# Optimization experiments

Measured on AMD Instinct MI355X. Metric: run time of the kernel, lower is better.

## Reference

```python
import jax, jax.numpy as jnp
import numpy as np

CHUNK = 32
NUM_HEADS = 4
HEAD_K = 256
HEAD_V = 256
EPS = 1e-05


def l2norm(x, eps=1e-6):
    return x * jax.lax.rsqrt(jnp.sum(x * x, axis=-1, keepdims=True) + eps)


def causal_depthwise_conv(x, w):
    # x: [b, l, d], w: [d, K]; causal depthwise conv1d (left pad K-1)
    K = w.shape[1]
    l = x.shape[1]
    xp = jnp.pad(x, ((0, 0), (K - 1, 0), (0, 0)))
    return sum(w[:, k] * xp[:, k:k + l, :] for k in range(K))


def delta_rule_chunkwise(q, k, v, beta):
    # q,k: [b,h,l,dk], v: [b,h,l,dv], beta: [b,h,l]; l divisible by CHUNK
    b, h, l, dk = q.shape
    dv = v.shape[-1]
    c = CHUNK
    n = l // c
    q = l2norm(q)
    k = l2norm(k)
    v = v * beta[..., None]
    k_beta = k * beta[..., None]
    resh = lambda x: x.reshape(b, h, n, c, x.shape[-1])
    q, k, v, k_beta = map(resh, (q, k, v, k_beta))
    tri_strict = jnp.tril(jnp.ones((c, c), dtype=q.dtype), -1)  # strictly lower
    attn = -(k_beta @ jnp.swapaxes(k, -1, -2)) * tri_strict  # [b,h,n,c,c]

    def body(i, a):
        # a[i, :i] += sum_j a[i, j] * a[j, :i]; zero elsewhere by structure
        row = a[..., i, :]  # [b,h,n,c]
        upd = jnp.einsum('bhnj,bhnjk->bhnk', row, a)
        return a.at[..., i, :].add(upd)

    attn = jax.lax.fori_loop(1, c, body, attn)
    attn = attn + jnp.eye(c, dtype=attn.dtype)
    u = attn @ v        # [b,h,n,c,dv]
    w = attn @ k_beta   # [b,h,n,c,dk]

    mask_causal = jnp.tril(jnp.ones((c, c), dtype=q.dtype), 0)  # incl diag
    S0 = jnp.zeros((b, h, dk, dv), dtype=q.dtype)
    to_front = lambda x: jnp.moveaxis(x, 2, 0)  # [n,b,h,c,d]

    def step(S, inp):
        q_i, k_i, u_i, w_i = inp
        attn_i = (q_i @ jnp.swapaxes(k_i, -1, -2)) * mask_causal
        u_new = u_i - w_i @ S
        o_i = q_i @ S + attn_i @ u_new
        S = S + jnp.swapaxes(k_i, -1, -2) @ u_new
        return S, o_i

    S, o = jax.lax.scan(step, S0, (to_front(q), to_front(k), to_front(u), to_front(w)))
    o = jnp.moveaxis(o, 0, 2).reshape(b, h, l, dv)
    return o, S


def setup_inputs() -> dict:
    key = jax.random.key(0)
    ks = jax.random.split(key, 12)
    b, l, d = 4, 4096, 1024
    sc = 0.02
    return {
        'hidden_states': jax.random.normal(ks[0], (b, l, d), jnp.float32),
        'Wq': jax.random.normal(ks[1], (1024, 1024), jnp.float32) * sc,
        'Wk': jax.random.normal(ks[2], (1024, 1024), jnp.float32) * sc,
        'Wv': jax.random.normal(ks[3], (1024, 1024), jnp.float32) * sc,
        'conv_q': jax.random.normal(ks[4], (1024, 4), jnp.float32) * 0.1,
        'conv_k': jax.random.normal(ks[5], (1024, 4), jnp.float32) * 0.1,
        'conv_v': jax.random.normal(ks[6], (1024, 4), jnp.float32) * 0.1,
        'Wb': jax.random.normal(ks[7], (4, 1024), jnp.float32) * sc,
        'Wmix': jax.random.normal(ks[8], (4, 1024), jnp.float32) * sc,
        'norm_w': jnp.ones((256,), jnp.float32),
        'Wo': jax.random.normal(ks[9], (1024, 1024), jnp.float32) * sc,
    }


def reference(hidden_states, Wq, Wk, Wv, conv_q, conv_k, conv_v, Wb, Wmix, norm_w, Wo):
    x = hidden_states
    b, l, d = x.shape
    h, dk, dv = NUM_HEADS, HEAD_K, HEAD_V
    # projections + depthwise causal short conv + silu
    q = jax.nn.silu(causal_depthwise_conv(x @ Wq.T, conv_q))
    k = jax.nn.silu(causal_depthwise_conv(x @ Wk.T, conv_k))
    v = jax.nn.silu(causal_depthwise_conv(x @ Wv.T, conv_v))
    v_token = v.reshape(b, l, h, dv)
    qh = q.reshape(b, l, h, dk).transpose(0, 2, 1, 3)
    kh = k.reshape(b, l, h, dk).transpose(0, 2, 1, 3)
    vh = v_token.transpose(0, 2, 1, 3)
    beta = jax.nn.sigmoid(x @ Wb.T).transpose(0, 2, 1)  # [b,h,l]
    o, S = delta_rule_chunkwise(qh, kh, vh, beta)
    o = o.transpose(0, 2, 1, 3)  # [b,l,h,dv]
    mix = jax.nn.sigmoid(x @ Wmix.T)[..., None]  # [b,l,h,1]
    o = mix * o + (1.0 - mix) * v_token
    # per-head RMSNorm
    o = o * jax.lax.rsqrt(jnp.mean(o * o, axis=-1, keepdims=True) + EPS) * norm_w
    o = o.reshape(b, l, h * dv) @ Wo.T
    return o
```

## Files before the change

kernel.cpp:

```cpp
#include <hip/hip_runtime.h>
#include <hip/hip_bf16.h>

typedef __hip_bfloat16 bf16;
typedef unsigned short u16;
typedef __attribute__((ext_vector_type(4))) float f32x4;
typedef __attribute__((ext_vector_type(8))) short bf16x8;
typedef __attribute__((ext_vector_type(2))) unsigned int u32x2;

#define MFMA16(a, b, c) __builtin_amdgcn_mfma_f32_16x16x32_bf16((a), (b), (c), 0, 0, 0)

__device__ __forceinline__ float bfu2f(u16 u){
  return __uint_as_float(((unsigned int)u) << 16);
}
__device__ __forceinline__ u16 f2bfu(float x){
  return __builtin_bit_cast(u16, __float2bfloat16(x));
}
__device__ __forceinline__ void gload16(const void* g, const void* l){
  __builtin_amdgcn_global_load_lds(
      (const __attribute__((address_space(1))) unsigned int*)g,
      (__attribute__((address_space(3))) unsigned int*)l, 16, 0, 0);
}

__global__ __launch_bounds__(256) void cvt_bf16(
    const float* __restrict__ src, u16* __restrict__ dst, int n8)
{
  int i = blockIdx.x * 256 + threadIdx.x;
  if (i >= n8) return;
  const float4* s = (const float4*)src;
  float4 a = s[i * 2], b = s[i * 2 + 1];
  u16 o[8] = {f2bfu(a.x), f2bfu(a.y), f2bfu(a.z), f2bfu(a.w),
              f2bfu(b.x), f2bfu(b.y), f2bfu(b.z), f2bfu(b.w)};
  *(bf16x8*)(dst + (size_t)i * 8) = *(bf16x8*)o;
}

template<int NMAT, bool F32OUT>
__global__ __launch_bounds__(256) void gemm_bt(
    const u16* __restrict__ A,
    const u16* __restrict__ B0, const u16* __restrict__ B1, const u16* __restrict__ B2,
    void* __restrict__ C0, void* __restrict__ C1, void* __restrict__ C2)
{
  const u16* B; void* C;
  if (NMAT == 1 || blockIdx.z == 0){ B = B0; C = C0; }
  else if (blockIdx.z == 1)        { B = B1; C = C1; }
  else                             { B = B2; C = C2; }
  __shared__ char lds[2][2][16384];
  const int tid = threadIdx.x;
  const int lane = tid & 63, wv = tid >> 6;
  const int lc = lane & 15, lh = lane >> 4;
  const int wr = wv >> 1, wc = wv & 1;
  const int m0 = blockIdx.x * 128, n0 = blockIdx.y * 128;

  f32x4 acc[4][4];
  #pragma unroll
  for (int mt = 0; mt < 4; mt++)
    #pragma unroll
    for (int nt = 0; nt < 4; nt++) acc[mt][nt] = (f32x4){0.f, 0.f, 0.f, 0.f};

  auto stage = [&](int buf, int k0){
    #pragma unroll
    for (int c = 0; c < 4; c++){
      const int q = wv * 4096 + c * 1024;
      const int row = (q >> 7) + (lane >> 3);
      const int slot = (lane & 7) ^ (row & 7);
      gload16(A + (size_t)(m0 + row) * 1024 + k0 + slot * 8, &lds[buf][0][q]);
      gload16(B + (size_t)(n0 + row) * 1024 + k0 + slot * 8, &lds[buf][1][q]);
    }
  };

  stage(0, 0);
  __syncthreads();
  int cur = 0;
  for (int t = 0; t < 16; t++){
    if (t < 15) stage(cur ^ 1, (t + 1) * 64);
    const char* Abuf = lds[cur][0];
    const char* Bbuf = lds[cur][1];
    #pragma unroll
    for (int kk = 0; kk < 2; kk++){
      bf16x8 af[4], bfr[4];
      #pragma unroll
      for (int mt = 0; mt < 4; mt++){
        int r = wr * 64 + mt * 16 + lc;
        int slot = (kk * 4 + lh) ^ (r & 7);
        af[mt] = *(const bf16x8*)(const void*)(Abuf + r * 128 + slot * 16);
      }
      #pragma unroll
      for (int nt = 0; nt < 4; nt++){
        int r = wc * 64 + nt * 16 + lc;
        int slot = (kk * 4 + lh) ^ (r & 7);
        bfr[nt] = *(const bf16x8*)(const void*)(Bbuf + r * 128 + slot * 16);
      }
      #pragma unroll
      for (int mt = 0; mt < 4; mt++)
        #pragma unroll
        for (int nt = 0; nt < 4; nt++)
          acc[mt][nt] = MFMA16(af[mt], bfr[nt], acc[mt][nt]);
    }
    __syncthreads();
    cur ^= 1;
  }

  #pragma unroll
  for (int mt = 0; mt < 4; mt++)
    #pragma unroll
    for (int nt = 0; nt < 4; nt++)
      #pragma unroll
      for (int rg = 0; rg < 4; rg++){
        int row = m0 + wr * 64 + mt * 16 + lh * 4 + rg;
        int col = n0 + wc * 64 + nt * 16 + lc;
        if (F32OUT) ((float*)C)[(size_t)row * 1024 + col] = acc[mt][nt][rg];
        else ((bf16*)C)[(size_t)row * 1024 + col] = __float2bfloat16(acc[mt][nt][rg]);
      }
}

__global__ __launch_bounds__(256) void small_proj(
    const float* __restrict__ x, const float* __restrict__ Wb,
    const float* __restrict__ Wmix, float* __restrict__ beta, float* __restrict__ mixb)
{
  const int tok = blockIdx.x;
  const int tid = threadIdx.x;
  __shared__ __align__(16) float xrow[1024];
  ((float4*)xrow)[tid] = ((const float4*)(x + (size_t)tok * 1024))[tid];
  __syncthreads();
  const int o = tid >> 5, g = tid & 31;
  const float* Wrow = (o < 4) ? (Wb + (size_t)o * 1024) : (Wmix + (size_t)(o - 4) * 1024);
  float p = 0.f;
  for (int e = g; e < 256; e += 32){
    float4 xv = ((const float4*)xrow)[e];
    float4 wv = ((const float4*)Wrow)[e];
    p += xv.x * wv.x + xv.y * wv.y + xv.z * wv.z + xv.w * wv.w;
  }
  for (int off = 16; off; off >>= 1) p += __shfl_down(p, off, 32);
  if (g == 0){
    float s = 1.f / (1.f + expf(-p));
    int b = tok >> 12, t = tok & 4095;
    if (o < 4) beta[((size_t)(b * 4 + o)) * 4096 + t] = s;
    else       mixb[(size_t)tok * 4 + (o - 4)] = s;
  }
}

__global__ __launch_bounds__(256) void conv_silu3(
    const bf16* __restrict__ in0, const bf16* __restrict__ in1, const bf16* __restrict__ in2,
    const float* __restrict__ w0, const float* __restrict__ w1, const float* __restrict__ w2,
    bf16* __restrict__ o0, bf16* __restrict__ o1, bf16* __restrict__ o2)
{
  const bf16* in; const float* wc; bf16* out;
  if (blockIdx.y == 0)      { in = in0; wc = w0; out = o0; }
  else if (blockIdx.y == 1) { in = in1; wc = w1; out = o1; }
  else                      { in = in2; wc = w2; out = o2; }
  const int idx8 = blockIdx.x * 256 + threadIdx.x;
  const int c8 = (idx8 & 127) * 8;
  const int tt = idx8 >> 7;
  const int t  = tt & 4095;
  const u16* inu = (const u16*)in;
  const size_t base = (size_t)tt * 1024 + c8;
  bf16x8 zv = {0, 0, 0, 0, 0, 0, 0, 0};
  bf16x8 x3 = *(const bf16x8*)(const void*)(inu + base);
  bf16x8 x2 = (t >= 1) ? *(const bf16x8*)(const void*)(inu + base - 1024) : zv;
  bf16x8 x1 = (t >= 2) ? *(const bf16x8*)(const void*)(inu + base - 2048) : zv;
  bf16x8 x0 = (t >= 3) ? *(const bf16x8*)(const void*)(inu + base - 3072) : zv;
  u16 o8[8];
  #pragma unroll
  for (int e = 0; e < 8; e++){
    const float4 w4 = ((const float4*)wc)[c8 + e];
    float s = w4.w * bfu2f((u16)x3[e]) + w4.z * bfu2f((u16)x2[e])
            + w4.y * bfu2f((u16)x1[e]) + w4.x * bfu2f((u16)x0[e]);
    s = s / (1.f + expf(-s));
    o8[e] = f2bfu(s);
  }
  *(bf16x8*)(void*)((u16*)out + base) = *(bf16x8*)o8;
}

__global__ __launch_bounds__(256, 2) void chunk_prep(
    bf16* __restrict__ qc, const bf16* __restrict__ kc, const bf16* __restrict__ vc,
    const float* __restrict__ beta,
    bf16* __restrict__ u_out, bf16* __restrict__ w_out,
    bf16* __restrict__ Ab, bf16* __restrict__ kTg)
{
  __shared__ char kS[16384], qS[16384];
  __shared__ float att[1056];
  __shared__ char Th[2048], Tl[2048];
  __shared__ char vTh[8192], vTl[8192];
  __shared__ char wTh[8192], wTl[8192];
  __shared__ float rnk_s[32], rnq_s[32], bvec[32];

  const int g = blockIdx.x;
  const int ch = g & 127, h = (g >> 7) & 3, b = g >> 9;
  const int tid = threadIdx.x;
  const int l = tid & 63, wv = tid >> 6;
  const int lc = l & 15, lh = l >> 4;
  const int i = tid >> 3, s = tid & 7;
  const size_t rowbase = ((size_t)(b * 4096 + ch * 32)) * 1024 + (size_t)h * 256;
  const u16* kcu = (const u16*)kc;
  const u16* qcu = (const u16*)qc;
  const u16* vcu = (const u16*)vc;

  bf16x8 kr[4], qr[4], vr[4];
  float ssk = 0.f, ssq = 0.f;
  #pragma unroll
  for (int j4 = 0; j4 < 4; j4++){
    size_t eo = rowbase + (size_t)i * 1024 + s * 32 + j4 * 8;
    kr[j4] = *(const bf16x8*)(const void*)(kcu + eo);
    qr[j4] = *(const bf16x8*)(const void*)(qcu + eo);
    vr[j4] = *(const bf16x8*)(const void*)(vcu + eo);
    #pragma unroll
    for (int e = 0; e < 8; e++){
      float kv = bfu2f((u16)kr[j4][e]); ssk += kv * kv;
      float qv = bfu2f((u16)qr[j4][e]); ssq += qv * qv;
    }
  }
  #pragma unroll
  for (int off = 1; off < 8; off <<= 1){
    ssk += __shfl_xor(ssk, off, 64);
    ssq += __shfl_xor(ssq, off, 64);
  }
  if (s == 0){
    rnk_s[i] = 1.0f / sqrtf(ssk + 1e-6f);
    rnq_s[i] = 1.0f / sqrtf(ssq + 1e-6f);
  }
  if (tid < 32) bvec[tid] = beta[((size_t)(b * 4 + h)) * 4096 + ch * 32 + tid];
  __syncthreads();

  const float rk = rnk_s[i], rq = rnq_s[i], bi = bvec[i];
  #pragma unroll
  for (int j4 = 0; j4 < 4; j4++){
    u16 kn8[8], qn8[8];
    #pragma unroll
    for (int e = 0; e < 8; e++){
      kn8[e] = f2bfu(bfu2f((u16)kr[j4][e]) * rk);
      qn8[e] = f2bfu(bfu2f((u16)qr[j4][e]) * rq);
    }
    int byt = (i * 512 + s * 64 + j4 * 16) ^ ((i & 7) << 4);
    *(bf16x8*)(void*)(kS + byt) = *(bf16x8*)kn8;
    *(bf16x8*)(void*)(qS + byt) = *(bf16x8*)qn8;
    *(bf16x8*)(void*)((u16*)qc + rowbase + (size_t)i * 1024 + s * 32 + j4 * 8) = *(bf16x8*)kn8 * 0 + *(bf16x8*)qn8;
  }
  if ((s >> 2) == 0){
    #pragma unroll
    for (int j4 = 0; j4 < 4; j4++)
      #pragma unroll
      for (int e = 0; e < 8; e++){
        int dl = (s & 3) * 32 + j4 * 8 + e;
        float vb = bfu2f((u16)vr[j4][e]) * bi;
        float kb = bfu2f((u16)kr[j4][e]) * rk * bi;
        u16 vh = f2bfu(vb), kh = f2bfu(kb);
        u16 vlo = f2bfu(vb - bfu2f(vh)), klo = f2bfu(kb - bfu2f(kh));
        int byt = dl * 64 + (((i >> 3) ^ ((dl >> 1) & 3)) << 4) + (i & 7) * 2;
        *(u16*)(vTh + byt) = vh; *(u16*)(vTl + byt) = vlo;
        *(u16*)(wTh + byt) = kh; *(u16*)(wTl + byt) = klo;
      }
  }
  __syncthreads();

  {
    const int mq = wv >> 1, nq = wv & 1;
    const int rowA = mq * 16 + lc, rowB = nq * 16 + lc;
    const int swA = (rowA & 7) << 4, swB = (rowB & 7) << 4;
    f32x4 accL = (f32x4){0.f, 0.f, 0.f, 0.f};
    f32x4 accA = (f32x4){0.f, 0.f, 0.f, 0.f};
    #pragma unroll
    for (int kt = 0; kt < 8; kt++){
      bf16x8 af  = *(const bf16x8*)(const void*)(kS + ((rowA * 512 + kt * 64 + lh * 16) ^ swA));
      bf16x8 bf_ = *(const bf16x8*)(const void*)(kS + ((rowB * 512 + kt * 64 + lh * 16) ^ swB));
      bf16x8 aq  = *(const bf16x8*)(const void*)(qS + ((rowA * 512 + kt * 64 + lh * 16) ^ swA));
      accL = MFMA16(af, bf_, accL);
      accA = MFMA16(aq, bf_, accA);
    }
    #pragma unroll
    for (int r = 0; r < 4; r++){
      int rr = mq * 16 + lh * 4 + r, cc = nq * 16 + lc;
      att[rr * 33 + cc] = (cc < rr) ? (-bvec[rr] * accL[r]) : 0.f;
      float av = (cc <= rr) ? accA[r] : 0.f;
      ((u16*)Ab)[(size_t)g * 1024 + rr * 32 + cc] = f2bfu(av);
    }
  }
  {
    u16 tmp[32];
    #pragma unroll
    for (int i2 = 0; i2 < 32; i2++)
      tmp[i2] = *(const u16*)(kS + ((i2 * 512 + tid * 2) ^ ((i2 & 7) << 4)));
    #pragma unroll
    for (int j4 = 0; j4 < 4; j4++)
      *(bf16x8*)(void*)((u16*)kTg + (size_t)g * 8192 + tid * 32 + j4 * 8) = *(bf16x8*)(tmp + j4 * 8);
  }
  __syncthreads();

  if (wv == 0 && l < 32){
    for (int ii = 1; ii < 32; ii++){
      float upd = 0.f;
      for (int m = 0; m < ii; m++)
        upd += att[ii * 33 + m] * att[m * 33 + l];
      att[ii * 33 + l] += upd;
    }
    att[l * 33 + l] = 1.0f;
  }
  __syncthreads();

  #pragma unroll
  for (int z = 0; z < 4; z++){
    int e = tid * 4 + z;
    int row = e >> 5, col = e & 31;
    float f = att[row * 33 + col];
    u16 hh = f2bfu(f), llo = f2bfu(f - bfu2f(hh));
    int byt = row * 64 + ((((col >> 3)) ^ ((row >> 1) & 3)) << 4) + (col & 7) * 2;
    *(u16*)(Th + byt) = hh; *(u16*)(Tl + byt) = llo;
  }
  __syncthreads();

  {
    const int mq = wv >> 1, nsel = wv & 1;
    const int rowA = mq * 16 + lc;
    const int sa = (lh ^ ((rowA >> 1) & 3)) << 4;
    bf16x8 ta = *(const bf16x8*)(const void*)(Th + rowA * 64 + sa);
    bf16x8 tl = *(const bf16x8*)(const void*)(Tl + rowA * 64 + sa);
    #pragma unroll
    for (int half = 0; half < 2; half++){
      if (half == 1){
        __syncthreads();
        if ((s >> 2) == 1){
          #pragma unroll
          for (int j4 = 0; j4 < 4; j4++)
            #pragma unroll
            for (int e = 0; e < 8; e++){
              int dl = (s & 3) * 32 + j4 * 8 + e;
              float vb = bfu2f((u16)vr[j4][e]) * bi;
              float kb = bfu2f((u16)kr[j4][e]) * rk * bi;
              u16 vh = f2bfu(vb), kh = f2bfu(kb);
              u16 vlo = f2bfu(vb - bfu2f(vh)), klo = f2bfu(kb - bfu2f(kh));
              int byt = dl * 64 + (((i >> 3) ^ ((dl >> 1) & 3)) << 4) + (i & 7) * 2;
              *(u16*)(vTh + byt) = vh; *(u16*)(vTl + byt) = vlo;
              *(u16*)(wTh + byt) = kh; *(u16*)(wTl + byt) = klo;
            }
        }
        __syncthreads();
      }
      #pragma unroll
      for (int nt = 0; nt < 4; nt++){
        int nl = nsel * 64 + nt * 16;
        int rowB = nl + lc;
        int sb = (lh ^ ((rowB >> 1) & 3)) << 4;
        bf16x8 bh_ = *(const bf16x8*)(const void*)(vTh + rowB * 64 + sb);
        bf16x8 bl_ = *(const bf16x8*)(const void*)(vTl + rowB * 64 + sb);
        f32x4 aU = (f32x4){0.f, 0.f, 0.f, 0.f};
        aU = MFMA16(ta, bh_, aU);
        aU = MFMA16(ta, bl_, aU);
        aU = MFMA16(tl, bh_, aU);
        bf16x8 wh_ = *(const bf16x8*)(const void*)(wTh + rowB * 64 + sb);
        bf16x8 wl_ = *(const bf16x8*)(const void*)(wTl + rowB * 64 + sb);
        f32x4 aW = (f32x4){0.f, 0.f, 0.f, 0.f};
        aW = MFMA16(ta, wh_, aW);
        aW = MFMA16(ta, wl_, aW);
        aW = MFMA16(tl, wh_, aW);
        #pragma unroll
        for (int r = 0; r < 4; r++){
          int row = mq * 16 + lh * 4 + r, col = half * 128 + nl + lc;
          ((u16*)u_out)[rowbase + (size_t)row * 1024 + col] = f2bfu(aU[r]);
          ((u16*)w_out)[rowbase + (size_t)row * 1024 + col] = f2bfu(aW[r]);
        }
      }
    }
  }
}

__global__ __launch_bounds__(128, 1) void scan_kernel(
    const u16* __restrict__ w_in, const u16* __restrict__ qn,
    const u16* __restrict__ u_in, const bf16* __restrict__ Ab,
    const bf16* __restrict__ kTg, bf16* __restrict__ o_out)
{
  extern __shared__ char smem[];
  char* wqbuf  = smem;
  char* stbuf  = smem + 65536;
  char* untbuf = smem + 81920;

  const int tid = threadIdx.x;
  const int l = tid & 63, wv = tid >> 6;
  const int lc = l & 15, lh = l >> 4;
  const int wg = blockIdx.x;
  const int bh = (wg & 7) * 2 + ((wg >> 3) & 1);
  const int vb = wg >> 4;
  const int h = bh & 3, b = bh >> 2;
  const int c0 = vb * 16;
  const int mw = wv * 16;

  f32x4 Sf[8];
  #pragma unroll
  for (int mt = 0; mt < 8; mt++) Sf[mt] = (f32x4){0.f, 0.f, 0.f, 0.f};

  const size_t bhElem = (size_t)b * 4096 * 1024 + (size_t)h * 256;
  const u16* kTu = (const u16*)kTg;

  auto stageWQ = [&](int buf, size_t rowE){
    char* wbase = wqbuf + buf * 32768 + wv * 8192;
    #pragma unroll
    for (int p = 0; p < 8; p++){
      int i = wv * 16 + p * 2 + (l >> 5);
      int logc = (l & 31) ^ (i & 7);
      size_t src = rowE + (size_t)i * 1024 + (size_t)logc * 8;
      gload16(w_in + src, wbase + p * 1024);
      gload16(qn  + src, wbase + 16384 + p * 1024);
    }
  };

  stageWQ(0, bhElem);
  for (int e = tid; e < 4096; e += 128) ((unsigned int*)(void*)stbuf)[e] = 0u;
  u16 cu0 = u_in[bhElem + (size_t)(mw + lh*4 + 0) * 1024 + c0 + lc];
  u16 cu1 = u_in[bhElem + (size_t)(mw + lh*4 + 1) * 1024 + c0 + lc];
  u16 cu2 = u_in[bhElem + (size_t)(mw + lh*4 + 2) * 1024 + c0 + lc];
  u16 cu3 = u_in[bhElem + (size_t)(mw + lh*4 + 3) * 1024 + c0 + lc];
  bf16x8 cAf = *(const bf16x8*)(const void*)(Ab + (size_t)(bh * 128) * 1024 + (mw + lc) * 32 + lh * 8);
  __syncthreads();

  int cur = 0;
  for (int ch = 0; ch < 128; ch++){
    const size_t rowElem = bhElem + (size_t)ch * 32768;
    if (ch < 127) stageWQ(cur ^ 1, rowElem + 32768);
    bf16x8 kF[8];
    {
      const size_t ktCur = (size_t)(bh * 128 + ch) * 8192;
      #pragma unroll
      for (int mt = 0; mt < 8; mt++){
        int rowK = wv * 128 + mt * 16 + lc;
        kF[mt] = *(const bf16x8*)(const void*)(kTu + ktCur + (size_t)rowK * 32 + lh * 8);
      }
    }
    u16 pu0, pu1, pu2, pu3; bf16x8 pAf;
    if (ch < 127){
      const size_t rowN = rowElem + 32768;
      pu0 = u_in[rowN + (size_t)(mw + lh*4 + 0) * 1024 + c0 + lc];
      pu1 = u_in[rowN + (size_t)(mw + lh*4 + 1) * 1024 + c0 + lc];
      pu2 = u_in[rowN + (size_t)(mw + lh*4 + 2) * 1024 + c0 + lc];
      pu3 = u_in[rowN + (size_t)(mw + lh*4 + 3) * 1024 + c0 + lc];
      pAf = *(const bf16x8*)(const void*)(Ab + (size_t)(bh * 128 + ch + 1) * 1024 + (mw + lc) * 32 + lh * 8);
    }

    const char* wl = wqbuf + cur * 32768;
    const char* ql = wl + 16384;

    f32x4 aU0 = (f32x4){0.f,0.f,0.f,0.f}, aU1 = (f32x4){0.f,0.f,0.f,0.f};
    f32x4 aO0 = (f32x4){0.f,0.f,0.f,0.f}, aO1 = (f32x4){0.f,0.f,0.f,0.f};
    {
      const int rowA = mw + lc;
      const int swA = (rowA & 7) << 4;
      const int swS = (lc & 7) << 4;
      #pragma unroll
      for (int kt = 0; kt < 8; kt++){
        const int kb = kt * 64 + lh * 16;
        bf16x8 aw = *(const bf16x8*)(const void*)(wl + ((rowA * 512 + kb) ^ swA));
        bf16x8 aq = *(const bf16x8*)(const void*)(ql + ((rowA * 512 + kb) ^ swA));
        bf16x8 sh = *(const bf16x8*)(const void*)(stbuf + ((lc * 512 + kb) ^ swS));
        bf16x8 sl = *(const bf16x8*)(const void*)(stbuf + 8192 + ((lc * 512 + kb) ^ swS));
        if (kt & 1){
          aU1 = MFMA16(aw, sh, aU1);
          aU1 = MFMA16(aw, sl, aU1);
          aO1 = MFMA16(aq, sh, aO1);
          aO1 = MFMA16(aq, sl, aO1);
        } else {
          aU0 = MFMA16(aw, sh, aU0);
          aU0 = MFMA16(aw, sl, aU0);
          aO0 = MFMA16(aq, sh, aO0);
          aO0 = MFMA16(aq, sl, aO0);
        }
      }
    }
    f32x4 accO = aO0 + aO1;
    {
      f32x4 accU = aU0 + aU1;
      float v0 = bfu2f(cu0) - accU[0];
      float v1 = bfu2f(cu1) - accU[1];
      float v2 = bfu2f(cu2) - accU[2];
      float v3 = bfu2f(cu3) - accU[3];
      u16 h0 = f2bfu(v0), h1 = f2bfu(v1), h2 = f2bfu(v2), h3 = f2bfu(v3);
      u16 l0 = f2bfu(v0 - bfu2f(h0)), l1 = f2bfu(v1 - bfu2f(h1));
      u16 l2 = f2bfu(v2 - bfu2f(h2)), l3 = f2bfu(v3 - bfu2f(h3));
      unsigned int ph0 = (unsigned)h0 | ((unsigned)h1 << 16), ph1 = (unsigned)h2 | ((unsigned)h3 << 16);
      unsigned int pl0 = (unsigned)l0 | ((unsigned)l1 << 16), pl1 = (unsigned)l2 | ((unsigned)l3 << 16);
      int off = lc * 80 + (mw + lh * 4) * 2;
      *(u32x2*)(void*)(untbuf + off)        = (u32x2){ph0, ph1};
      *(u32x2*)(void*)(untbuf + 1280 + off) = (u32x2){pl0, pl1};
    }
    __syncthreads();

    bf16x8 uh = *(const bf16x8*)(const void*)(untbuf + lc * 80 + lh * 16);
    bf16x8 ul = *(const bf16x8*)(const void*)(untbuf + 1280 + lc * 80 + lh * 16);
    accO = MFMA16(cAf, uh, accO);
    accO = MFMA16(cAf, ul, accO);
    o_out[rowElem + (size_t)(mw + lh*4 + 0) * 1024 + c0 + lc] = __float2bfloat16(accO[0]);
    o_out[rowElem + (size_t)(mw + lh*4 + 1) * 1024 + c0 + lc] = __float2bfloat16(accO[1]);
    o_out[rowElem + (size_t)(mw + lh*4 + 2) * 1024 + c0 + lc] = __float2bfloat16(accO[2]);
    o_out[rowElem + (size_t)(mw + lh*4 + 3) * 1024 + c0 + lc] = __float2bfloat16(accO[3]);

    #pragma unroll
    for (int mt = 0; mt < 8; mt++){
      Sf[mt] = MFMA16(kF[mt], uh, Sf[mt]);
      Sf[mt] = MFMA16(kF[mt], ul, Sf[mt]);
    }

    #pragma unroll
    for (int mt = 0; mt < 8; mt++){
      const int dbase = wv * 128 + mt * 16 + lh * 4;
      float v0 = Sf[mt][0], v1 = Sf[mt][1], v2 = Sf[mt][2], v3 = Sf[mt][3];
      u16 h0 = f2bfu(v0), h1 = f2bfu(v1), h2 = f2bfu(v2), h3 = f2bfu(v3);
      u16 s0 = f2bfu(v0 - bfu2f(h0)), s1 = f2bfu(v1 - bfu2f(h1));
      u16 s2 = f2bfu(v2 - bfu2f(h2)), s3 = f2bfu(v3 - bfu2f(h3));
      int off = ((lc * 512 + dbase * 2) ^ ((lc & 7) << 4));
      *(u32x2*)(void*)(stbuf + off) =
          (u32x2){(unsigned)h0 | ((unsigned)h1 << 16), (unsigned)h2 | ((unsigned)h3 << 16)};
      *(u32x2*)(void*)(stbuf + 8192 + off) =
          (u32x2){(unsigned)s0 | ((unsigned)s1 << 16), (unsigned)s2 | ((unsigned)s3 << 16)};
    }
    if (ch < 127){
      cu0 = pu0; cu1 = pu1; cu2 = pu2; cu3 = pu3; cAf = pAf;
    }
    __syncthreads();
    cur ^= 1;
  }
}

__global__ __launch_bounds__(256) void postproc(
    const bf16* __restrict__ o_in, const bf16* __restrict__ v_tok,
    const float* __restrict__ mixb, const float* __restrict__ norm_w,
    bf16* __restrict__ onorm)
{
  const int blk = blockIdx.x;
  const int d = threadIdx.x;
  const size_t gg = (size_t)blk * 256 + d;
  float ov = __bfloat162float(o_in[gg]);
  float vv = __bfloat162float(v_tok[gg]);
  float m = mixb[blk];
  float val = m * ov + (1.f - m) * vv;
  float ss = val * val;
  for (int off = 32; off; off >>= 1) ss += __shfl_down(ss, off, 64);
  __shared__ float wsum[4];
  if ((d & 63) == 0) wsum[d >> 6] = ss;
  __syncthreads();
  float tot = wsum[0] + wsum[1] + wsum[2] + wsum[3];
  float r = rsqrtf(tot * (1.f / 256.f) + 1e-5f);
  onorm[gg] = __float2bfloat16(val * r * norm_w[d]);
}

extern "C" void kernel_launch(void* const* d_in, const int* in_sizes, int n_in,
                              void* d_out, int out_size, void* d_ws, size_t ws_size,
                              hipStream_t stream)
{
  (void)in_sizes; (void)n_in; (void)out_size; (void)ws_size;
  const float* x     = (const float*)d_in[0];
  const float* Wq    = (const float*)d_in[1];
  const float* Wk    = (const float*)d_in[2];
  const float* Wv    = (const float*)d_in[3];
  const float* convq = (const float*)d_in[4];
  const float* convk = (const float*)d_in[5];
  const float* convv = (const float*)d_in[6];
  const float* Wb    = (const float*)d_in[7];
  const float* Wmix  = (const float*)d_in[8];
  const float* normw = (const float*)d_in[9];
  const float* Wo    = (const float*)d_in[10];
  float* out = (float*)d_out;

  char* wsb = (char*)d_ws;
  const size_t BIGB = (size_t)16777216 * 2;
  bf16* b0 = (bf16*)(wsb + 0*BIGB);
  bf16* b1 = (bf16*)(wsb + 1*BIGB);
  bf16* b2 = (bf16*)(wsb + 2*BIGB);
  bf16* b3 = (bf16*)(wsb + 3*BIGB);
  bf16* b4 = (bf16*)(wsb + 4*BIGB);
  bf16* b5 = (bf16*)(wsb + 5*BIGB);
  bf16*  Ab   = (bf16*) (wsb + 6*BIGB);
  float* beta = (float*)(wsb + 6*BIGB + 4194304);
  float* mixb = beta + 65536;
  bf16*  kTg  = (bf16*) (wsb + 6*BIGB + 4194304 + 524288);

  u16* xbf = (u16*)b4;
  u16* wqb = (u16*)b3;
  u16* wkb = wqb + (size_t)1024*1024;
  u16* wvb = wkb + (size_t)1024*1024;
  u16* wob = (u16*)kTg;

  cvt_bf16<<<8192, 256, 0, stream>>>(x, xbf, 2097152);
  cvt_bf16<<<512, 256, 0, stream>>>(Wq, wqb, 131072);
  cvt_bf16<<<512, 256, 0, stream>>>(Wk, wkb, 131072);
  cvt_bf16<<<512, 256, 0, stream>>>(Wv, wvb, 131072);

  gemm_bt<3, false><<<dim3(128, 8, 3), 256, 0, stream>>>(
      xbf, wqb, wkb, wvb, (void*)b0, (void*)b1, (void*)b2);
  small_proj<<<16384, 256, 0, stream>>>(x, Wb, Wmix, beta, mixb);
  conv_silu3<<<dim3(8192, 3), 256, 0, stream>>>(
      b0, b1, b2, convq, convk, convv, b3, b4, b5);
  chunk_prep<<<2048, 256, 0, stream>>>(b3, b4, b5, beta, b2, b0, Ab, kTg);
  hipFuncSetAttribute((const void*)scan_kernel,
                      hipFuncAttributeMaxDynamicSharedMemorySize, 84480);
  scan_kernel<<<256, 128, 84480, stream>>>((const u16*)b0, (const u16*)b3,
                                           (const u16*)b2, Ab, kTg, b1);
  cvt_bf16<<<512, 256, 0, stream>>>(Wo, wob, 131072);
  postproc  <<<65536, 256, 0, stream>>>(b1, b5, mixb, normw, b3);
  gemm_bt<1, true><<<dim3(128, 8, 1), 256, 0, stream>>>(
      (const u16*)b3, wob, wob, wob, (void*)out, (void*)out, (void*)out);
}
```

Baseline: 660.0 us.

## Repartition scan kernel: each wave owns 8 value columns with full state

The chunk scan now launches 64 workgroups of 8 waves instead of 256 workgroups of 2 waves. Each wave owns an 8-column slice of the value dimension and keeps the full 256-row state slice in registers, staging its state in a private LDS region. This removes the mid-chunk block barrier that exchanged u_new between waves; only the end-of-chunk barrier remains. In exchange, half of each 16-wide MFMA tile is wasted on padding (lanes with lc>=8 are idle) and register pressure doubles. Fewer workgroups also means far fewer CUs are used.

```diff
diff --git a/kernel.cpp b/kernel.cpp
--- a/kernel.cpp
+++ b/kernel.cpp
@@ -361,154 +361,178 @@
   }
 }
 
-__global__ __launch_bounds__(128, 1) void scan_kernel(
+__global__ __launch_bounds__(512, 2) void scan_kernel(
     const u16* __restrict__ w_in, const u16* __restrict__ qn,
     const u16* __restrict__ u_in, const bf16* __restrict__ Ab,
     const bf16* __restrict__ kTg, bf16* __restrict__ o_out)
 {
   extern __shared__ char smem[];
-  char* wqbuf  = smem;
-  char* stbuf  = smem + 65536;
-  char* untbuf = smem + 81920;
+  char* wqbuf = smem;
+  char* stbuf = smem + 65536;
+  char* unbuf = smem + 135168;
 
   const int tid = threadIdx.x;
   const int l = tid & 63, wv = tid >> 6;
   const int lc = l & 15, lh = l >> 4;
   const int wg = blockIdx.x;
   const int bh = (wg & 7) * 2 + ((wg >> 3) & 1);
-  const int vb = wg >> 4;
+  const int qb = wg >> 4;
   const int h = bh & 3, b = bh >> 2;
-  const int c0 = vb * 16;
-  const int mw = wv * 16;
-
-  f32x4 Sf[8];
-  #pragma unroll
-  for (int mt = 0; mt < 8; mt++) Sf[mt] = (f32x4){0.f, 0.f, 0.f, 0.f};
+  const int c0 = qb * 64 + wv * 8;
+
+  char* stw = stbuf + wv * 8704;
+  char* unw = unbuf + wv * 1280;
+
+  f32x4 Sf[16];
+  #pragma unroll
+  for (int mt = 0; mt < 16; mt++) Sf[mt] = (f32x4){0.f, 0.f, 0.f, 0.f};
 
   const size_t bhElem = (size_t)b * 4096 * 1024 + (size_t)h * 256;
   const u16* kTu = (const u16*)kTg;
 
   auto stageWQ = [&](int buf, size_t rowE){
-    char* wbase = wqbuf + buf * 32768 + wv * 8192;
-    #pragma unroll
-    for (int p = 0; p < 8; p++){
-      int i = wv * 16 + p * 2 + (l >> 5);
-      int logc = (l & 31) ^ (i & 7);
+    char* base = wqbuf + buf * 32768;
+    #pragma unroll
+    for (int s2 = 0; s2 < 2; s2++){
+      const int seg = wv * 2 + s2;
+      const int i = seg * 2 + (l >> 5);
+      const int logc = (l & 31) ^ (i & 7);
       size_t src = rowE + (size_t)i * 1024 + (size_t)logc * 8;
-      gload16(w_in + src, wbase + p * 1024);
-      gload16(qn  + src, wbase + 16384 + p * 1024);
+      gload16(w_in + src, base + seg * 1024);
+      gload16(qn  + src, base + 16384 + seg * 1024);
     }
   };
 
   stageWQ(0, bhElem);
-  for (int e = tid; e < 4096; e += 128) ((unsigned int*)(void*)stbuf)[e] = 0u;
-  u16 cu0 = u_in[bhElem + (size_t)(mw + lh*4 + 0) * 1024 + c0 + lc];
-  u16 cu1 = u_in[bhElem + (size_t)(mw + lh*4 + 1) * 1024 + c0 + lc];
-  u16 cu2 = u_in[bhElem + (size_t)(mw + lh*4 + 2) * 1024 + c0 + lc];
-  u16 cu3 = u_in[bhElem + (size_t)(mw + lh*4 + 3) * 1024 + c0 + lc];
-  bf16x8 cAf = *(const bf16x8*)(const void*)(Ab + (size_t)(bh * 128) * 1024 + (mw + lc) * 32 + lh * 8);
+  for (int e = tid; e < 19968; e += 512) ((unsigned int*)(void*)stbuf)[e] = 0u;
+  u16 cu[2][4]; bf16x8 cAf[2];
+  #pragma unroll
+  for (int mb = 0; mb < 2; mb++){
+    #pragma unroll
+    for (int r = 0; r < 4; r++)
+      cu[mb][r] = u_in[bhElem + (size_t)(mb*16 + lh*4 + r) * 1024 + c0 + (lc & 7)];
+    cAf[mb] = *(const bf16x8*)(const void*)(Ab + (size_t)(bh * 128) * 1024 + (mb*16 + lc) * 32 + lh * 8);
+  }
   __syncthreads();
 
   int cur = 0;
   for (int ch = 0; ch < 128; ch++){
     const size_t rowElem = bhElem + (size_t)ch * 32768;
-    if (ch < 127) stageWQ(cur ^ 1, rowElem + 32768);
-    bf16x8 kF[8];
+    u16 pu[2][4]; bf16x8 pAf[2];
+    if (ch < 127){
+      const size_t rowN = rowElem + 32768;
+      stageWQ(cur ^ 1, rowN);
+      #pragma unroll
+      for (int mb = 0; mb < 2; mb++){
+        #pragma unroll
+        for (int r = 0; r < 4; r++)
+          pu[mb][r] = u_in[rowN + (size_t)(mb*16 + lh*4 + r) * 1024 + c0 + (lc & 7)];
+        pAf[mb] = *(const bf16x8*)(const void*)(Ab + (size_t)(bh * 128 + ch + 1) * 1024 + (mb*16 + lc) * 32 + lh * 8);
+      }
+    }
+
+    const char* wl = wqbuf + cur * 32768;
+    const char* ql = wl + 16384;
+
+    f32x4 accU[2], accO[2];
+    #pragma unroll
+    for (int mb = 0; mb < 2; mb++){
+      accU[mb] = (f32x4){0.f,0.f,0.f,0.f};
+      accO[mb] = (f32x4){0.f,0.f,0.f,0.f};
+    }
+    {
+      const int colS = lc & 7;
+      #pragma unroll
+      for (int kt = 0; kt < 8; kt++){
+        const int dby = (kt * 64 + lh * 16) ^ (colS << 4);
+        bf16x8 sh = *(const bf16x8*)(const void*)(stw + colS * 544 + dby);
+        bf16x8 sl = *(const bf16x8*)(const void*)(stw + 4352 + colS * 544 + dby);
+        #pragma unroll
+        for (int mb = 0; mb < 2; mb++){
+          const int rowA = mb * 16 + lc;
+          const int swA = (rowA & 7) << 4;
+          bf16x8 aw = *(const bf16x8*)(const void*)(wl + ((rowA * 512 + kt * 64 + lh * 16) ^ swA));
+          bf16x8 aq = *(const bf16x8*)(const void*)(ql + ((rowA * 512 + kt * 64 + lh * 16) ^ swA));
+          accU[mb] = MFMA16(aw, sh, accU[mb]);
+          accU[mb] = MFMA16(aw, sl, accU[mb]);
+          accO[mb] = MFMA16(aq, sh, accO[mb]);
+          accO[mb] = MFMA16(aq, sl, accO[mb]);
+        }
+      }
+    }
+    if (lc < 8){
+      #pragma unroll
+      for (int mb = 0; mb < 2; mb++){
+        float v0 = bfu2f(cu[mb][0]) - accU[mb][0];
+        float v1 = bfu2f(cu[mb][1]) - accU[mb][1];
+        float v2 = bfu2f(cu[mb][2]) - accU[mb][2];
+        float v3 = bfu2f(cu[mb][3]) - accU[mb][3];
+        u16 h0 = f2bfu(v0), h1 = f2bfu(v1), h2 = f2bfu(v2), h3 = f2bfu(v3);
+        u16 l0 = f2bfu(v0 - bfu2f(h0)), l1 = f2bfu(v1 - bfu2f(h1));
+        u16 l2 = f2bfu(v2 - bfu2f(h2)), l3 = f2bfu(v3 - bfu2f(h3));
+        int off = lc * 80 + (mb * 16 + lh * 4) * 2;
+        *(u32x2*)(void*)(unw + off) =
+            (u32x2){(unsigned)h0 | ((unsigned)h1 << 16), (unsigned)h2 | ((unsigned)h3 << 16)};
+        *(u32x2*)(void*)(unw + 640 + off) =
+            (u32x2){(unsigned)l0 | ((unsigned)l1 << 16), (unsigned)l2 | ((unsigned)l3 << 16)};
+      }
+    }
+    asm volatile("" ::: "memory");
+    bf16x8 uh = *(const bf16x8*)(const void*)(unw + (lc & 7) * 80 + lh * 16);
+    bf16x8 ul = *(const bf16x8*)(const void*)(unw + 640 + (lc & 7) * 80 + lh * 16);
+
+    #pragma unroll
+    for (int mb = 0; mb < 2; mb++){
+      accO[mb] = MFMA16(cAf[mb], uh, accO[mb]);
+      accO[mb] = MFMA16(cAf[mb], ul, accO[mb]);
+    }
+    if (lc < 8){
+      #pragma unroll
+      for (int mb = 0; mb < 2; mb++)
+        #pragma unroll
+        for (int r = 0; r < 4; r++)
+          o_out[rowElem + (size_t)(mb*16 + lh*4 + r) * 1024 + c0 + lc] = __float2bfloat16(accO[mb][r]);
+    }
+
     {
       const size_t ktCur = (size_t)(bh * 128 + ch) * 8192;
       #pragma unroll
-      for (int mt = 0; mt < 8; mt++){
-        int rowK = wv * 128 + mt * 16 + lc;
-        kF[mt] = *(const bf16x8*)(const void*)(kTu + ktCur + (size_t)rowK * 32 + lh * 8);
-      }
-    }
-    u16 pu0, pu1, pu2, pu3; bf16x8 pAf;
+      for (int half = 0; half < 2; half++){
+        bf16x8 kF[8];
+        #pragma unroll
+        for (int mt = 0; mt < 8; mt++){
+          int rowK = half * 128 + mt * 16 + lc;
+          kF[mt] = *(const bf16x8*)(const void*)(kTu + ktCur + (size_t)rowK * 32 + lh * 8);
+        }
+        #pragma unroll
+        for (int mt = 0; mt < 8; mt++){
+          Sf[half*8 + mt] = MFMA16(kF[mt], uh, Sf[half*8 + mt]);
+          Sf[half*8 + mt] = MFMA16(kF[mt], ul, Sf[half*8 + mt]);
+        }
+      }
+    }
+
+    if (lc < 8){
+      #pragma unroll
+      for (int mt = 0; mt < 16; mt++){
+        float v0 = Sf[mt][0], v1 = Sf[mt][1], v2 = Sf[mt][2], v3 = Sf[mt][3];
+        u16 h0 = f2bfu(v0), h1 = f2bfu(v1), h2 = f2bfu(v2), h3 = f2bfu(v3);
+        u16 s0 = f2bfu(v0 - bfu2f(h0)), s1 = f2bfu(v1 - bfu2f(h1));
+        u16 s2 = f2bfu(v2 - bfu2f(h2)), s3 = f2bfu(v3 - bfu2f(h3));
+        int dby = (mt * 32 + lh * 8) ^ (lc << 4);
+        *(u32x2*)(void*)(stw + lc * 544 + dby) =
+            (u32x2){(unsigned)h0 | ((unsigned)h1 << 16), (unsigned)h2 | ((unsigned)h3 << 16)};
+        *(u32x2*)(void*)(stw + 4352 + lc * 544 + dby) =
+            (u32x2){(unsigned)s0 | ((unsigned)s1 << 16), (unsigned)s2 | ((unsigned)s3 << 16)};
+      }
+    }
     if (ch < 127){
-      const size_t rowN = rowElem + 32768;
-      pu0 = u_in[rowN + (size_t)(mw + lh*4 + 0) * 1024 + c0 + lc];
-      pu1 = u_in[rowN + (size_t)(mw + lh*4 + 1) * 1024 + c0 + lc];
-      pu2 = u_in[rowN + (size_t)(mw + lh*4 + 2) * 1024 + c0 + lc];
-      pu3 = u_in[rowN + (size_t)(mw + lh*4 + 3) * 1024 + c0 + lc];
-      pAf = *(const bf16x8*)(const void*)(Ab + (size_t)(bh * 128 + ch + 1) * 1024 + (mw + lc) * 32 + lh * 8);
-    }
-
-    const char* wl = wqbuf + cur * 32768;
-    const char* ql = wl + 16384;
-
-    f32x4 aU0 = (f32x4){0.f,0.f,0.f,0.f}, aU1 = (f32x4){0.f,0.f,0.f,0.f};
-    f32x4 aO0 = (f32x4){0.f,0.f,0.f,0.f}, aO1 = (f32x4){0.f,0.f,0.f,0.f};
-    {
-      const int rowA = mw + lc;
-      const int swA = (rowA & 7) << 4;
-      const int swS = (lc & 7) << 4;
-      #pragma unroll
-      for (int kt = 0; kt < 8; kt++){
-        const int kb = kt * 64 + lh * 16;
-        bf16x8 aw = *(const bf16x8*)(const void*)(wl + ((rowA * 512 + kb) ^ swA));
-        bf16x8 aq = *(const bf16x8*)(const void*)(ql + ((rowA * 512 + kb) ^ swA));
-        bf16x8 sh = *(const bf16x8*)(const void*)(stbuf + ((lc * 512 + kb) ^ swS));
-        bf16x8 sl = *(const bf16x8*)(const void*)(stbuf + 8192 + ((lc * 512 + kb) ^ swS));
-        if (kt & 1){
-          aU1 = MFMA16(aw, sh, aU1);
-          aU1 = MFMA16(aw, sl, aU1);
-          aO1 = MFMA16(aq, sh, aO1);
-          aO1 = MFMA16(aq, sl, aO1);
-        } else {
-          aU0 = MFMA16(aw, sh, aU0);
-          aU0 = MFMA16(aw, sl, aU0);
-          aO0 = MFMA16(aq, sh, aO0);
-          aO0 = MFMA16(aq, sl, aO0);
-        }
-      }
-    }
-    f32x4 accO = aO0 + aO1;
-    {
-      f32x4 accU = aU0 + aU1;
-      float v0 = bfu2f(cu0) - accU[0];
-      float v1 = bfu2f(cu1) - accU[1];
-      float v2 = bfu2f(cu2) - accU[2];
-      float v3 = bfu2f(cu3) - accU[3];
-      u16 h0 = f2bfu(v0), h1 = f2bfu(v1), h2 = f2bfu(v2), h3 = f2bfu(v3);
-      u16 l0 = f2bfu(v0 - bfu2f(h0)), l1 = f2bfu(v1 - bfu2f(h1));
-      u16 l2 = f2bfu(v2 - bfu2f(h2)), l3 = f2bfu(v3 - bfu2f(h3));
-      unsigned int ph0 = (unsigned)h0 | ((unsigned)h1 << 16), ph1 = (unsigned)h2 | ((unsigned)h3 << 16);
-      unsigned int pl0 = (unsigned)l0 | ((unsigned)l1 << 16), pl1 = (unsigned)l2 | ((unsigned)l3 << 16);
-      int off = lc * 80 + (mw + lh * 4) * 2;
-      *(u32x2*)(void*)(untbuf + off)        = (u32x2){ph0, ph1};
-      *(u32x2*)(void*)(untbuf + 1280 + off) = (u32x2){pl0, pl1};
-    }
-    __syncthreads();
-
-    bf16x8 uh = *(const bf16x8*)(const void*)(untbuf + lc * 80 + lh * 16);
-    bf16x8 ul = *(const bf16x8*)(const void*)(untbuf + 1280 + lc * 80 + lh * 16);
-    accO = MFMA16(cAf, uh, accO);
-    accO = MFMA16(cAf, ul, accO);
-    o_out[rowElem + (size_t)(mw + lh*4 + 0) * 1024 + c0 + lc] = __float2bfloat16(accO[0]);
-    o_out[rowElem + (size_t)(mw + lh*4 + 1) * 1024 + c0 + lc] = __float2bfloat16(accO[1]);
-    o_out[rowElem + (size_t)(mw + lh*4 + 2) * 1024 + c0 + lc] = __float2bfloat16(accO[2]);
-    o_out[rowElem + (size_t)(mw + lh*4 + 3) * 1024 + c0 + lc] = __float2bfloat16(accO[3]);
-
-    #pragma unroll
-    for (int mt = 0; mt < 8; mt++){
-      Sf[mt] = MFMA16(kF[mt], uh, Sf[mt]);
-      Sf[mt] = MFMA16(kF[mt], ul, Sf[mt]);
-    }
-
-    #pragma unroll
-    for (int mt = 0; mt < 8; mt++){
-      const int dbase = wv * 128 + mt * 16 + lh * 4;
-      float v0 = Sf[mt][0], v1 = Sf[mt][1], v2 = Sf[mt][2], v3 = Sf[mt][3];
-      u16 h0 = f2bfu(v0), h1 = f2bfu(v1), h2 = f2bfu(v2), h3 = f2bfu(v3);
-      u16 s0 = f2bfu(v0 - bfu2f(h0)), s1 = f2bfu(v1 - bfu2f(h1));
-      u16 s2 = f2bfu(v2 - bfu2f(h2)), s3 = f2bfu(v3 - bfu2f(h3));
-      int off = ((lc * 512 + dbase * 2) ^ ((lc & 7) << 4));
-      *(u32x2*)(void*)(stbuf + off) =
-          (u32x2){(unsigned)h0 | ((unsigned)h1 << 16), (unsigned)h2 | ((unsigned)h3 << 16)};
-      *(u32x2*)(void*)(stbuf + 8192 + off) =
-          (u32x2){(unsigned)s0 | ((unsigned)s1 << 16), (unsigned)s2 | ((unsigned)s3 << 16)};
-    }
-    if (ch < 127){
-      cu0 = pu0; cu1 = pu1; cu2 = pu2; cu3 = pu3; cAf = pAf;
+      #pragma unroll
+      for (int mb = 0; mb < 2; mb++){
+        #pragma unroll
+        for (int r = 0; r < 4; r++) cu[mb][r] = pu[mb][r];
+        cAf[mb] = pAf[mb];
+      }
     }
     __syncthreads();
     cur ^= 1;
@@ -586,8 +610,8 @@
       b0, b1, b2, convq, convk, convv, b3, b4, b5);
   chunk_prep<<<2048, 256, 0, stream>>>(b3, b4, b5, beta, b2, b0, Ab, kTg);
   hipFuncSetAttribute((const void*)scan_kernel,
-                      hipFuncAttributeMaxDynamicSharedMemorySize, 84480);
-  scan_kernel<<<256, 128, 84480, stream>>>((const u16*)b0, (const u16*)b3,
+                      hipFuncAttributeMaxDynamicSharedMemorySize, 145408);
+  scan_kernel<<<64, 512, 145408, stream>>>((const u16*)b0, (const u16*)b3,
                                            (const u16*)b2, Ab, kTg, b1);
   cvt_bf16<<<512, 256, 0, stream>>>(Wo, wob, 131072);
   postproc  <<<65536, 256, 0, stream>>>(b1, b5, mixb, normw, b3);
```

Result: slower. 1.071 ms (+62.2%).
